# Optimization experiments

Measured on AMD Instinct MI355X. Metric: run time of the kernel, lower is better.

Reference implementation:

```python
import jax, jax.numpy as jnp
import numpy as np

B, T, C, H = 4, 4096, 512, 64

def setup_inputs() -> dict:
    key = jax.random.key(0)
    ks = jax.random.split(key, 9)
    k = jax.random.normal(ks[0], (B, T, C), dtype=jnp.float32)
    v = jax.random.normal(ks[1], (B, T, C), dtype=jnp.float32)
    q = jax.random.normal(ks[2], (B, T, C), dtype=jnp.float32)
    # causal lower-triangular mask, positions with 0 are masked to -inf
    mask = jnp.tril(jnp.ones((T, T), dtype=jnp.int32))
    s = 1.0 / np.sqrt(C)
    kW = jax.random.normal(ks[3], (C, H), dtype=jnp.float32) * s
    kb = jax.random.normal(ks[4], (H,), dtype=jnp.float32) * s
    vW = jax.random.normal(ks[5], (C, H), dtype=jnp.float32) * s
    vb = jax.random.normal(ks[6], (H,), dtype=jnp.float32) * s
    qW = jax.random.normal(ks[7], (C, H), dtype=jnp.float32) * s
    qb = jax.random.normal(ks[8], (H,), dtype=jnp.float32) * s
    return {"k": k, "v": v, "q": q, "mask": mask,
            "kW": kW, "kb": kb, "vW": vW, "vb": vb, "qW": qW, "qb": qb}

def reference(k, v, q, mask, kW, kb, vW, vb, qW, qb):
    C_in = k.shape[-1]
    kp = k @ kW + kb                              # [B,T,H]
    qp = q @ qW + qb                              # [B,T,H]
    # NOTE: original scales by embedding_size**-0.5 (C), not head_size**-0.5
    attn = jnp.einsum('bth,bsh->bts', qp, kp) * (C_in ** -0.5)  # [B,T,T]
    attn = jnp.where(mask[None, :, :] == 0, -jnp.inf, attn)
    attn = jax.nn.softmax(attn, axis=-1)
    vp = v @ vW + vb                              # [B,T,H]
    out = attn @ vp                               # [B,T,H]
    return out
```

## Files before the change

### kernel.cpp

```cpp
#include <hip/hip_runtime.h>
#include <hip/hip_bf16.h>

#define Bq 4
#define Tq 4096
#define Cq 512
#define Hq 64
#define NEG_BIG (-3.0e38f)

using bf16   = __bf16;
using bf16x8 = __attribute__((ext_vector_type(8))) __bf16;
using bf16x4 = __attribute__((ext_vector_type(4))) __bf16;
using f32x4  = __attribute__((ext_vector_type(4))) float;
using f32x16 = __attribute__((ext_vector_type(16))) float;

static __device__ __forceinline__ float other_half_f(float x) {
    return __shfl_xor(x, 32, 64);
}
static __device__ __forceinline__ unsigned other_half_u(unsigned x) {
    return (unsigned)__shfl_xor((int)x, 32, 64);
}
static __device__ __forceinline__ unsigned pk2(float x, float y) {
    union { bf16 h[2]; unsigned u; } t;
    t.h[0] = (bf16)x; t.h[1] = (bf16)y;
    return t.u;
}
union W8 { unsigned u[4]; bf16x8 v; };

#define BUILD_B(p, BA, BB) do {                                                \
    const unsigned w0 = pk2(p[0],  p[1]),  w1 = pk2(p[2],  p[3]);              \
    const unsigned w2 = pk2(p[4],  p[5]),  w3 = pk2(p[6],  p[7]);              \
    const unsigned w4 = pk2(p[8],  p[9]),  w5 = pk2(p[10], p[11]);             \
    const unsigned w6 = pk2(p[12], p[13]), w7 = pk2(p[14], p[15]);             \
    const unsigned o0 = other_half_u(w0), o1 = other_half_u(w1);               \
    const unsigned o2 = other_half_u(w2), o3 = other_half_u(w3);               \
    const unsigned o4 = other_half_u(w4), o5 = other_half_u(w5);               \
    const unsigned o6 = other_half_u(w6), o7 = other_half_u(w7);               \
    BA.u[0] = hi ? o2 : w0;  BA.u[1] = hi ? o3 : w1;                           \
    BA.u[2] = hi ? w2 : o0;  BA.u[3] = hi ? w3 : o1;                           \
    BB.u[0] = hi ? o6 : w4;  BB.u[1] = hi ? o7 : w5;                           \
    BB.u[2] = hi ? w6 : o4;  BB.u[3] = hi ? w7 : o5;                           \
} while (0)

__global__ __launch_bounds__(256) void prep_weights_kernel(
    const float* __restrict__ kW, const float* __restrict__ qW,
    const float* __restrict__ vW, bf16* __restrict__ WT)
{
    int i = blockIdx.x * 256 + threadIdx.x;
    int t = i >> 15;
    int r = i & 32767;
    int h = r >> 9;
    int c = r & 511;
    const float* W = (t == 0) ? kW : (t == 1) ? qW : vW;
    WT[i] = (bf16)W[c * Hq + h];
}

__global__ __launch_bounds__(256) void proj_kernel(
    const float* __restrict__ Xk, const float* __restrict__ Xq,
    const float* __restrict__ Xv, const bf16* __restrict__ WT,
    const float* __restrict__ bk, const float* __restrict__ bq,
    const float* __restrict__ bv,
    bf16* __restrict__ kp, bf16* __restrict__ qp, bf16* __restrict__ vpT)
{
    const int t    = blockIdx.y;
    const int lane = threadIdx.x & 63;
    const int wave = threadIdx.x >> 6;
    const int lq   = lane & 15;
    const int lg   = lane >> 4;
    const int row0 = blockIdx.x * 64 + wave * 16;

    const float* X    = (t == 0) ? Xk : (t == 1) ? Xq : Xv;
    const float* bias = (t == 0) ? bk : (t == 1) ? bq : bv;
    const bf16*  Wt   = WT + (size_t)t * (Hq * Cq);

    const float* Xrow = X + (size_t)(row0 + lq) * Cq + lg * 8;

    f32x4 acc[4];
#pragma unroll
    for (int i = 0; i < 4; ++i) acc[i] = f32x4{0.f, 0.f, 0.f, 0.f};

#pragma unroll 4
    for (int kc = 0; kc < Cq; kc += 32) {
        float4 a0 = *(const float4*)(Xrow + kc);
        float4 a1 = *(const float4*)(Xrow + kc + 4);
        bf16x8 af;
        af[0] = (bf16)a0.x; af[1] = (bf16)a0.y; af[2] = (bf16)a0.z; af[3] = (bf16)a0.w;
        af[4] = (bf16)a1.x; af[5] = (bf16)a1.y; af[6] = (bf16)a1.z; af[7] = (bf16)a1.w;
#pragma unroll
        for (int ht = 0; ht < 4; ++ht) {
            bf16x8 bfB = *(const bf16x8*)(Wt + (size_t)(ht * 16 + lq) * Cq + kc + lg * 8);
            acc[ht] = __builtin_amdgcn_mfma_f32_16x16x32_bf16(af, bfB, acc[ht], 0, 0, 0);
        }
    }

    const float scale = (t == 1) ? (0.044194173824159216f * 1.4426950408889634f) : 1.0f;

    if (t < 2) {
        bf16* dst = (t == 0) ? kp : qp;
#pragma unroll
        for (int ht = 0; ht < 4; ++ht) {
            float bb = bias[ht * 16 + lq];
#pragma unroll
            for (int r = 0; r < 4; ++r) {
                int row = row0 + 4 * lg + r;
                dst[(size_t)row * Hq + ht * 16 + lq] = (bf16)((acc[ht][r] + bb) * scale);
            }
        }
    } else {
#pragma unroll
        for (int ht = 0; ht < 4; ++ht) {
            float bb = bias[ht * 16 + lq];
            bf16x4 pk;
#pragma unroll
            for (int r = 0; r < 4; ++r) pk[r] = (bf16)(acc[ht][r] + bb);
            int rowg = row0 + 4 * lg;
            int bidx = rowg >> 12;
            int tt   = rowg & 4095;
            int h    = ht * 16 + lq;
            *(bf16x4*)(vpT + (((size_t)(bidx * Hq + h)) << 12) + tt) = pk;
        }
    }
}

__global__ __launch_bounds__(256, 2) void attn_kernel(
    const bf16* __restrict__ qp, const bf16* __restrict__ kp,
    const bf16* __restrict__ vpT,
    bf16* __restrict__ PO, float* __restrict__ PML)
{
    __shared__ char lds_raw[2][16384];

    const int x = blockIdx.x;
    const int b = x & 3;
    const int j = 31 - ((x >> 2) & 31);
    const int c = x >> 7;
    const int kstart = c * 512;
    const int klim   = (j + 1) * 128;
    if (kstart >= klim) return;
    const int kend = min(kstart + 512, klim);
    const int nt   = (kend - kstart) >> 6;

    const int tid  = threadIdx.x;
    const int wid  = tid >> 6;
    const int lane = tid & 63;
    const int l31  = lane & 31;
    const int half = lane >> 5;
    const bool hi  = half != 0;
    const int qt   = j * 4 + wid;
    const int qb   = qt * 32;
    const int qg   = qb + l31;
    const int qlast = qb + 31;

    const bf16* kp_b = kp  + (size_t)b * Tq * Hq;
    const bf16* vp_b = vpT + (size_t)b * Hq * Tq;

    const int srow = tid >> 2;
    const int sseg = (tid & 3) * 16;
    const int sswz = (srow & 7) << 4;

#define STAGE_LOAD(T, r0, r1, r2, r3) do {                                     \
    const int k0_ = kstart + (T) * 64;                                         \
    const bf16* kg_ = kp_b + (size_t)(k0_ + srow) * Hq + (sseg >> 1);          \
    r0 = *(const int4*)(kg_);                                                  \
    r1 = *(const int4*)(kg_ + 32);                                             \
    const bf16* vg_ = vp_b + (size_t)srow * Tq + k0_ + (sseg >> 1);            \
    r2 = *(const int4*)(vg_);                                                  \
    r3 = *(const int4*)(vg_ + 32);                                             \
} while (0)

#define STAGE_WRITE(BUF, r0, r1, r2, r3) do {                                  \
    char* base_ = lds_raw[BUF];                                                \
    *(int4*)(base_ + srow * 128 + (sseg ^ sswz))          = r0;                \
    *(int4*)(base_ + srow * 128 + ((sseg + 64) ^ sswz))   = r1;                \
    *(int4*)(base_ + 8192 + srow * 128 + (sseg ^ sswz))        = r2;           \
    *(int4*)(base_ + 8192 + srow * 128 + ((sseg + 64) ^ sswz)) = r3;           \
} while (0)

    const bf16* qrow = qp + ((size_t)b * Tq + qb + l31) * Hq + half * 8;
    const bf16x8 Q0 = *(const bf16x8*)(qrow);
    const bf16x8 Q1 = *(const bf16x8*)(qrow + 16);
    const bf16x8 Q2 = *(const bf16x8*)(qrow + 32);
    const bf16x8 Q3 = *(const bf16x8*)(qrow + 48);

    f32x16 O0, O1;
#pragma unroll
    for (int r = 0; r < 16; ++r) { O0[r] = 0.f; O1[r] = 0.f; }
    float l = 0.f;

    const int rswz = (l31 & 7) << 4;
    const int cb   = half * 16;

    int4 s0, s1, s2, s3;
    STAGE_LOAD(0, s0, s1, s2, s3);
    STAGE_WRITE(0, s0, s1, s2, s3);
    __syncthreads();

    int cur = 0;
    for (int t = 0; t < nt; ++t) {
        const bool more = (t + 1 < nt);
        if (more) STAGE_LOAD(t + 1, s0, s1, s2, s3);

        const int k0t = kstart + t * 64;
        if (k0t <= qlast) {
            const char* base = lds_raw[cur];
            const char* kr0 = base + l31 * 128;
            const char* kr1 = base + (32 + l31) * 128;
            const char* vr0 = base + 8192 + l31 * 128;
            const char* vr1 = base + 8192 + (32 + l31) * 128;

            const bf16x8 K00 = *(const bf16x8*)(kr0 + ((cb +  0) ^ rswz));
            const bf16x8 K01 = *(const bf16x8*)(kr0 + ((cb + 32) ^ rswz));
            const bf16x8 K02 = *(const bf16x8*)(kr0 + ((cb + 64) ^ rswz));
            const bf16x8 K03 = *(const bf16x8*)(kr0 + ((cb + 96) ^ rswz));
            const bf16x8 K10 = *(const bf16x8*)(kr1 + ((cb +  0) ^ rswz));
            const bf16x8 K11 = *(const bf16x8*)(kr1 + ((cb + 32) ^ rswz));
            const bf16x8 K12 = *(const bf16x8*)(kr1 + ((cb + 64) ^ rswz));
            const bf16x8 K13 = *(const bf16x8*)(kr1 + ((cb + 96) ^ rswz));
            const bf16x8 Vh0k0 = *(const bf16x8*)(vr0 + ((cb +  0) ^ rswz));
            const bf16x8 Vh0k1 = *(const bf16x8*)(vr0 + ((cb + 32) ^ rswz));
            const bf16x8 Vh0k2 = *(const bf16x8*)(vr0 + ((cb + 64) ^ rswz));
            const bf16x8 Vh0k3 = *(const bf16x8*)(vr0 + ((cb + 96) ^ rswz));
            const bf16x8 Vh1k0 = *(const bf16x8*)(vr1 + ((cb +  0) ^ rswz));
            const bf16x8 Vh1k1 = *(const bf16x8*)(vr1 + ((cb + 32) ^ rswz));
            const bf16x8 Vh1k2 = *(const bf16x8*)(vr1 + ((cb + 64) ^ rswz));
            const bf16x8 Vh1k3 = *(const bf16x8*)(vr1 + ((cb + 96) ^ rswz));

            f32x16 S0, S1;
#pragma unroll
            for (int r = 0; r < 16; ++r) { S0[r] = 0.f; S1[r] = 0.f; }
            S0 = __builtin_amdgcn_mfma_f32_32x32x16_bf16(K00, Q0, S0, 0, 0, 0);
            S1 = __builtin_amdgcn_mfma_f32_32x32x16_bf16(K10, Q0, S1, 0, 0, 0);
            S0 = __builtin_amdgcn_mfma_f32_32x32x16_bf16(K01, Q1, S0, 0, 0, 0);
            S1 = __builtin_amdgcn_mfma_f32_32x32x16_bf16(K11, Q1, S1, 0, 0, 0);
            S0 = __builtin_amdgcn_mfma_f32_32x32x16_bf16(K02, Q2, S0, 0, 0, 0);
            S1 = __builtin_amdgcn_mfma_f32_32x32x16_bf16(K12, Q2, S1, 0, 0, 0);
            S0 = __builtin_amdgcn_mfma_f32_32x32x16_bf16(K03, Q3, S0, 0, 0, 0);
            S1 = __builtin_amdgcn_mfma_f32_32x32x16_bf16(K13, Q3, S1, 0, 0, 0);

            if (k0t + 63 > qb) {
#pragma unroll
                for (int r = 0; r < 16; ++r) {
                    const int kg = k0t + (r & 3) + 8 * (r >> 2) + 4 * half;
                    if (kg > qg)      S0[r] = NEG_BIG;
                    if (kg + 32 > qg) S1[r] = NEG_BIG;
                }
            }

            float p0[16], p1[16];
#pragma unroll
            for (int r = 0; r < 16; ++r) {
                p0[r] = exp2f(S0[r]);
                p1[r] = exp2f(S1[r]);
            }
            l += (((p0[0]+p0[1])+(p0[2]+p0[3])) + ((p0[4]+p0[5])+(p0[6]+p0[7])))
               + (((p0[8]+p0[9])+(p0[10]+p0[11])) + ((p0[12]+p0[13])+(p0[14]+p0[15])))
               + (((p1[0]+p1[1])+(p1[2]+p1[3])) + ((p1[4]+p1[5])+(p1[6]+p1[7])))
               + (((p1[8]+p1[9])+(p1[10]+p1[11])) + ((p1[12]+p1[13])+(p1[14]+p1[15])));

            W8 B00, B01, B10, B11;
            BUILD_B(p0, B00, B01);
            BUILD_B(p1, B10, B11);

            O0 = __builtin_amdgcn_mfma_f32_32x32x16_bf16(Vh0k0, B00.v, O0, 0, 0, 0);
            O1 = __builtin_amdgcn_mfma_f32_32x32x16_bf16(Vh1k0, B00.v, O1, 0, 0, 0);
            O0 = __builtin_amdgcn_mfma_f32_32x32x16_bf16(Vh0k1, B01.v, O0, 0, 0, 0);
            O1 = __builtin_amdgcn_mfma_f32_32x32x16_bf16(Vh1k1, B01.v, O1, 0, 0, 0);
            O0 = __builtin_amdgcn_mfma_f32_32x32x16_bf16(Vh0k2, B10.v, O0, 0, 0, 0);
            O1 = __builtin_amdgcn_mfma_f32_32x32x16_bf16(Vh1k2, B10.v, O1, 0, 0, 0);
            O0 = __builtin_amdgcn_mfma_f32_32x32x16_bf16(Vh0k3, B11.v, O0, 0, 0, 0);
            O1 = __builtin_amdgcn_mfma_f32_32x32x16_bf16(Vh1k3, B11.v, O1, 0, 0, 0);
        }

        __syncthreads();
        if (more) STAGE_WRITE(cur ^ 1, s0, s1, s2, s3);
        __syncthreads();
        cur ^= 1;
    }
#undef STAGE_LOAD
#undef STAGE_WRITE

    const float ltot = l + other_half_f(l);
    const float inv  = (ltot > 0.f) ? (1.0f / ltot) : 0.f;
    const size_t slot = ((size_t)(b * 128 + qt)) * 8 + c;
    bf16* po = PO + slot * 2048;
#pragma unroll
    for (int r = 0; r < 16; ++r) {
        const int h = (r & 3) + 8 * (r >> 2) + 4 * half;
        po[h * 32 + l31]        = (bf16)(O0[r] * inv);
        po[(h + 32) * 32 + l31] = (bf16)(O1[r] * inv);
    }
    if (lane < 32) {
        PML[slot * 32 + l31] = ltot;
    }
}

__global__ __launch_bounds__(256) void combine_kernel(
    const bf16* __restrict__ PO, const float* __restrict__ PML,
    float* __restrict__ out)
{
    const int gid = blockIdx.x;
    const int b   = gid & 3;
    const int qt  = gid >> 2;
    const int qb  = qt * 32;
    const int nch = ((qt >> 2) + 4) >> 2;
    const size_t slot0 = ((size_t)(b * 128 + qt)) * 8;
    const int tid = threadIdx.x;
    const int q   = tid & 31;
    const int hh  = tid >> 5;

    float L = 0.f;
    float acc[8];
#pragma unroll
    for (int i = 0; i < 8; ++i) acc[i] = 0.f;

    for (int c = 0; c < nch; ++c) {
        const float w = PML[(slot0 + c) * 32 + q];
        L += w;
        const bf16* po = PO + (slot0 + c) * 2048;
#pragma unroll
        for (int ih = 0; ih < 8; ++ih)
            acc[ih] += w * (float)po[(hh + 8 * ih) * 32 + q];
    }
    const float inv = 1.0f / L;
#pragma unroll
    for (int ih = 0; ih < 8; ++ih)
        out[((size_t)b * Tq + qb + q) * Hq + hh + 8 * ih] = acc[ih] * inv;
}

extern "C" void kernel_launch(void* const* d_in, const int* in_sizes, int n_in,
                              void* d_out, int out_size, void* d_ws, size_t ws_size,
                              hipStream_t stream)
{
    const float* k  = (const float*)d_in[0];
    const float* v  = (const float*)d_in[1];
    const float* q  = (const float*)d_in[2];
    const float* kW = (const float*)d_in[4];
    const float* kb = (const float*)d_in[5];
    const float* vW = (const float*)d_in[6];
    const float* vb = (const float*)d_in[7];
    const float* qW = (const float*)d_in[8];
    const float* qb = (const float*)d_in[9];
    float* out = (float*)d_out;

    char* ws = (char*)d_ws;
    bf16*  WT  = (bf16*)(ws);
    bf16*  kp  = (bf16*)(ws + 196608);
    bf16*  qp  = (bf16*)(ws + 196608 + 2097152);
    bf16*  vpT = (bf16*)(ws + 196608 + 2 * 2097152);
    bf16*  PO  = (bf16*)(ws + 196608 + 3 * 2097152);
    float* PML = (float*)(ws + 196608 + 3 * 2097152 + 16777216);

    hipLaunchKernelGGL(prep_weights_kernel, dim3(384), dim3(256), 0, stream,
                       kW, qW, vW, WT);
    hipLaunchKernelGGL(proj_kernel, dim3(256, 3), dim3(256), 0, stream,
                       k, q, v, WT, kb, qb, vb, kp, qp, vpT);
    hipLaunchKernelGGL(attn_kernel, dim3(1024), dim3(256), 0, stream,
                       qp, kp, vpT, PO, PML);
    hipLaunchKernelGGL(combine_kernel, dim3(512), dim3(256), 0, stream,
                       PO, PML, out);
}
```

Measured before the change: 82.62 us.

## Stage projection inputs in swizzled LDS with coalesced loads, split heads across waves

The projection kernel now loads a 32-row tile of X with fully coalesced float4 reads, converts it to bf16 and stores it in XOR-swizzled shared memory. Each wave then reads its A fragments from LDS and computes only two of the four 16-column head tiles, and the grid doubles to 512 blocks per input. The weight-transpose prep kernel is also changed to read W contiguously and scatter the writes. This targets the strided global reads of X in the old projection and raises parallelism, at the cost of a barrier and 32KB of LDS per block.

New measurement: 82.94 us. Within noise of the previous version (+0.4%).

```diff
diff --git a/kernel.cpp b/kernel.cpp
--- a/kernel.cpp
+++ b/kernel.cpp
@@ -48,10 +48,10 @@
     int i = blockIdx.x * 256 + threadIdx.x;
     int t = i >> 15;
     int r = i & 32767;
-    int h = r >> 9;
-    int c = r & 511;
+    int c = r >> 6;
+    int h = r & 63;
     const float* W = (t == 0) ? kW : (t == 1) ? qW : vW;
-    WT[i] = (bf16)W[c * Hq + h];
+    WT[(size_t)t * 32768 + h * 512 + c] = (bf16)W[r];
 }
 
 __global__ __launch_bounds__(256) void proj_kernel(
@@ -61,61 +61,80 @@
     const float* __restrict__ bv,
     bf16* __restrict__ kp, bf16* __restrict__ qp, bf16* __restrict__ vpT)
 {
-    const int t    = blockIdx.y;
-    const int lane = threadIdx.x & 63;
-    const int wave = threadIdx.x >> 6;
-    const int lq   = lane & 15;
-    const int lg   = lane >> 4;
-    const int row0 = blockIdx.x * 64 + wave * 16;
-
+    __shared__ bf16 Xs[32 * 512];
+
+    const int t = blockIdx.y;
     const float* X    = (t == 0) ? Xk : (t == 1) ? Xq : Xv;
     const float* bias = (t == 0) ? bk : (t == 1) ? bq : bv;
     const bf16*  Wt   = WT + (size_t)t * (Hq * Cq);
 
-    const float* Xrow = X + (size_t)(row0 + lq) * Cq + lg * 8;
-
-    f32x4 acc[4];
-#pragma unroll
-    for (int i = 0; i < 4; ++i) acc[i] = f32x4{0.f, 0.f, 0.f, 0.f};
-
-#pragma unroll 4
-    for (int kc = 0; kc < Cq; kc += 32) {
-        float4 a0 = *(const float4*)(Xrow + kc);
-        float4 a1 = *(const float4*)(Xrow + kc + 4);
+    const int tid     = threadIdx.x;
+    const int row_blk = blockIdx.x * 32;
+    const float* Xb   = X + (size_t)row_blk * Cq;
+    char* lds = (char*)Xs;
+
+#pragma unroll
+    for (int i = 0; i < 8; ++i) {
+        const int idx = i * 2048 + tid * 8;
+        float4 a0 = *(const float4*)(Xb + idx);
+        float4 a1 = *(const float4*)(Xb + idx + 4);
         bf16x8 af;
         af[0] = (bf16)a0.x; af[1] = (bf16)a0.y; af[2] = (bf16)a0.z; af[3] = (bf16)a0.w;
         af[4] = (bf16)a1.x; af[5] = (bf16)a1.y; af[6] = (bf16)a1.z; af[7] = (bf16)a1.w;
-#pragma unroll
-        for (int ht = 0; ht < 4; ++ht) {
-            bf16x8 bfB = *(const bf16x8*)(Wt + (size_t)(ht * 16 + lq) * Cq + kc + lg * 8);
-            acc[ht] = __builtin_amdgcn_mfma_f32_16x16x32_bf16(af, bfB, acc[ht], 0, 0, 0);
-        }
+        const int row  = idx >> 9;
+        const int colB = (idx & 511) * 2;
+        *(bf16x8*)(lds + row * 1024 + (colB ^ ((row & 7) << 4))) = af;
+    }
+    __syncthreads();
+
+    const int lane = tid & 63;
+    const int wave = tid >> 6;
+    const int lq   = lane & 15;
+    const int lg   = lane >> 4;
+    const int rloc = (wave >> 1) * 16 + lq;
+    const int htb  = (wave & 1) * 2;
+    const char* arow = lds + rloc * 1024;
+    const int rswz   = (rloc & 7) << 4;
+
+    f32x4 acc0 = f32x4{0.f, 0.f, 0.f, 0.f};
+    f32x4 acc1 = f32x4{0.f, 0.f, 0.f, 0.f};
+
+#pragma unroll
+    for (int kc = 0; kc < Cq; kc += 32) {
+        const int colB = (kc + lg * 8) * 2;
+        bf16x8 af = *(const bf16x8*)(arow + (colB ^ rswz));
+        bf16x8 b0 = *(const bf16x8*)(Wt + (size_t)((htb * 16)      + lq) * Cq + kc + lg * 8);
+        bf16x8 b1 = *(const bf16x8*)(Wt + (size_t)((htb * 16 + 16) + lq) * Cq + kc + lg * 8);
+        acc0 = __builtin_amdgcn_mfma_f32_16x16x32_bf16(af, b0, acc0, 0, 0, 0);
+        acc1 = __builtin_amdgcn_mfma_f32_16x16x32_bf16(af, b1, acc1, 0, 0, 0);
     }
 
     const float scale = (t == 1) ? (0.044194173824159216f * 1.4426950408889634f) : 1.0f;
+    const int rowg = row_blk + (wave >> 1) * 16 + 4 * lg;
 
     if (t < 2) {
         bf16* dst = (t == 0) ? kp : qp;
 #pragma unroll
-        for (int ht = 0; ht < 4; ++ht) {
-            float bb = bias[ht * 16 + lq];
-#pragma unroll
-            for (int r = 0; r < 4; ++r) {
-                int row = row0 + 4 * lg + r;
-                dst[(size_t)row * Hq + ht * 16 + lq] = (bf16)((acc[ht][r] + bb) * scale);
-            }
+        for (int hh = 0; hh < 2; ++hh) {
+            const f32x4 a = hh ? acc1 : acc0;
+            const int ht = htb + hh;
+            const float bb = bias[ht * 16 + lq];
+#pragma unroll
+            for (int r = 0; r < 4; ++r)
+                dst[(size_t)(rowg + r) * Hq + ht * 16 + lq] = (bf16)((a[r] + bb) * scale);
         }
     } else {
-#pragma unroll
-        for (int ht = 0; ht < 4; ++ht) {
-            float bb = bias[ht * 16 + lq];
+        const int bidx = rowg >> 12;
+        const int tt   = rowg & 4095;
+#pragma unroll
+        for (int hh = 0; hh < 2; ++hh) {
+            const f32x4 a = hh ? acc1 : acc0;
+            const int ht = htb + hh;
+            const float bb = bias[ht * 16 + lq];
             bf16x4 pk;
 #pragma unroll
-            for (int r = 0; r < 4; ++r) pk[r] = (bf16)(acc[ht][r] + bb);
-            int rowg = row0 + 4 * lg;
-            int bidx = rowg >> 12;
-            int tt   = rowg & 4095;
-            int h    = ht * 16 + lq;
+            for (int r = 0; r < 4; ++r) pk[r] = (bf16)(a[r] + bb);
+            const int h = ht * 16 + lq;
             *(bf16x4*)(vpT + (((size_t)(bidx * Hq + h)) << 12) + tt) = pk;
         }
     }
@@ -350,7 +369,7 @@
 
     hipLaunchKernelGGL(prep_weights_kernel, dim3(384), dim3(256), 0, stream,
                        kW, qW, vW, WT);
-    hipLaunchKernelGGL(proj_kernel, dim3(256, 3), dim3(256), 0, stream,
+    hipLaunchKernelGGL(proj_kernel, dim3(512, 3), dim3(256), 0, stream,
                        k, q, v, WT, kb, qb, vb, kp, qp, vpT);
     hipLaunchKernelGGL(attn_kernel, dim3(1024), dim3(256), 0, stream,
                        qp, kp, vpT, PO, PML);
```

## Split projection across waves by head tile and coalesce weight transpose reads

Applied to the files above, without the earlier changes.

The projection kernel now gives each wave one 16-column head tile for a shared 16-row block, instead of each wave computing all four head tiles for its own 16 rows. The grid grows from 256 to 1024 blocks per tensor, which raises parallelism and cuts per-wave accumulator registers. The cost is that all four waves in a block load the same X rows, so X reads are repeated within a block, though they may hit in cache. The weight-prep kernel now reads W coalesced and scatters the transposed writes.

After: 120.6 us. +46.0%, slower.

```diff
diff --git a/kernel.cpp b/kernel.cpp
--- a/kernel.cpp
+++ b/kernel.cpp
@@ -48,10 +48,10 @@
     int i = blockIdx.x * 256 + threadIdx.x;
     int t = i >> 15;
     int r = i & 32767;
-    int h = r >> 9;
-    int c = r & 511;
+    int c = r >> 6;
+    int h = r & 63;
     const float* W = (t == 0) ? kW : (t == 1) ? qW : vW;
-    WT[i] = (bf16)W[c * Hq + h];
+    WT[(size_t)t * 32768 + h * 512 + c] = (bf16)W[r];
 }
 
 __global__ __launch_bounds__(256) void proj_kernel(
@@ -63,20 +63,19 @@
 {
     const int t    = blockIdx.y;
     const int lane = threadIdx.x & 63;
-    const int wave = threadIdx.x >> 6;
+    const int ht   = threadIdx.x >> 6;
     const int lq   = lane & 15;
     const int lg   = lane >> 4;
-    const int row0 = blockIdx.x * 64 + wave * 16;
+    const int row0 = blockIdx.x * 16;
 
     const float* X    = (t == 0) ? Xk : (t == 1) ? Xq : Xv;
     const float* bias = (t == 0) ? bk : (t == 1) ? bq : bv;
     const bf16*  Wt   = WT + (size_t)t * (Hq * Cq);
 
     const float* Xrow = X + (size_t)(row0 + lq) * Cq + lg * 8;
-
-    f32x4 acc[4];
-#pragma unroll
-    for (int i = 0; i < 4; ++i) acc[i] = f32x4{0.f, 0.f, 0.f, 0.f};
+    const bf16*  Wrow = Wt + (size_t)(ht * 16 + lq) * Cq + lg * 8;
+
+    f32x4 acc = f32x4{0.f, 0.f, 0.f, 0.f};
 
 #pragma unroll 4
     for (int kc = 0; kc < Cq; kc += 32) {
@@ -85,39 +84,29 @@
         bf16x8 af;
         af[0] = (bf16)a0.x; af[1] = (bf16)a0.y; af[2] = (bf16)a0.z; af[3] = (bf16)a0.w;
         af[4] = (bf16)a1.x; af[5] = (bf16)a1.y; af[6] = (bf16)a1.z; af[7] = (bf16)a1.w;
-#pragma unroll
-        for (int ht = 0; ht < 4; ++ht) {
-            bf16x8 bfB = *(const bf16x8*)(Wt + (size_t)(ht * 16 + lq) * Cq + kc + lg * 8);
-            acc[ht] = __builtin_amdgcn_mfma_f32_16x16x32_bf16(af, bfB, acc[ht], 0, 0, 0);
-        }
+        bf16x8 bfB = *(const bf16x8*)(Wrow + kc);
+        acc = __builtin_amdgcn_mfma_f32_16x16x32_bf16(af, bfB, acc, 0, 0, 0);
     }
 
     const float scale = (t == 1) ? (0.044194173824159216f * 1.4426950408889634f) : 1.0f;
+    const float bb = bias[ht * 16 + lq];
 
     if (t < 2) {
         bf16* dst = (t == 0) ? kp : qp;
 #pragma unroll
-        for (int ht = 0; ht < 4; ++ht) {
-            float bb = bias[ht * 16 + lq];
-#pragma unroll
-            for (int r = 0; r < 4; ++r) {
-                int row = row0 + 4 * lg + r;
-                dst[(size_t)row * Hq + ht * 16 + lq] = (bf16)((acc[ht][r] + bb) * scale);
-            }
+        for (int r = 0; r < 4; ++r) {
+            int row = row0 + 4 * lg + r;
+            dst[(size_t)row * Hq + ht * 16 + lq] = (bf16)((acc[r] + bb) * scale);
         }
     } else {
-#pragma unroll
-        for (int ht = 0; ht < 4; ++ht) {
-            float bb = bias[ht * 16 + lq];
-            bf16x4 pk;
-#pragma unroll
-            for (int r = 0; r < 4; ++r) pk[r] = (bf16)(acc[ht][r] + bb);
-            int rowg = row0 + 4 * lg;
-            int bidx = rowg >> 12;
-            int tt   = rowg & 4095;
-            int h    = ht * 16 + lq;
-            *(bf16x4*)(vpT + (((size_t)(bidx * Hq + h)) << 12) + tt) = pk;
-        }
+        bf16x4 pk;
+#pragma unroll
+        for (int r = 0; r < 4; ++r) pk[r] = (bf16)(acc[r] + bb);
+        int rowg = row0 + 4 * lg;
+        int bidx = rowg >> 12;
+        int tt   = rowg & 4095;
+        int h    = ht * 16 + lq;
+        *(bf16x4*)(vpT + (((size_t)(bidx * Hq + h)) << 12) + tt) = pk;
     }
 }
 
@@ -350,7 +339,7 @@
 
     hipLaunchKernelGGL(prep_weights_kernel, dim3(384), dim3(256), 0, stream,
                        kW, qW, vW, WT);
-    hipLaunchKernelGGL(proj_kernel, dim3(256, 3), dim3(256), 0, stream,
+    hipLaunchKernelGGL(proj_kernel, dim3(1024, 3), dim3(256), 0, stream,
                        k, q, v, WT, kb, qb, vb, kp, qp, vpT);
     hipLaunchKernelGGL(attn_kernel, dim3(1024), dim3(256), 0, stream,
                        qp, kp, vpT, PO, PML);
```
